# Optimization experiments

Measured on AMD Instinct MI355X. Metric: run time of the kernel, lower is better.

## Reference

```python
import jax, jax.numpy as jnp
import numpy as np

CHUNK = 32  # config.scan_chunk_size


def setup_inputs() -> dict:
    key = jax.random.key(0)
    ks = jax.random.split(key, 12)
    B, T, D, SD, OD = 8, 2048, 512, 256, 64
    w = lambda i, shape: (jax.random.normal(ks[i], shape, dtype=jnp.float32) * 0.02)
    return {
        "x": jax.random.normal(ks[0], (B, T, D), dtype=jnp.float32),
        "gate_W": w(1, (D, SD)), "gate_b": jnp.zeros((SD,), jnp.float32),
        "in_W": w(2, (D, SD)), "in_b": jnp.zeros((SD,), jnp.float32),
        "out_W": w(3, (SD, D)), "out_b": jnp.zeros((D,), jnp.float32),
        "opv_W": w(4, (D, OD)), "opv_b": jnp.zeros((OD,), jnp.float32),
        "opk_W": w(5, (D, OD)), "opk_b": jnp.zeros((OD,), jnp.float32),
        "opq_W": w(6, (D, OD)), "opq_b": jnp.zeros((OD,), jnp.float32),
        "op_decay": jnp.full((OD,), 0.95, jnp.float32),
        "opout_W": w(7, (OD, D)), "opout_b": jnp.zeros((D,), jnp.float32),
        "ln_g": jnp.ones((D,), jnp.float32), "ln_b": jnp.zeros((D,), jnp.float32),
    }


def _chunked_scan(gates, drive, K):
    # gates, drive: [B,T,SD]; T divisible by K
    B, T, SD = drive.shape
    nC = T // K
    a = gates.reshape(B, nC, K, SD)
    b = drive.reshape(B, nC, K, SD)
    log_cum_a = jnp.cumsum(jnp.log(jnp.maximum(a, 1e-6)), axis=2)
    cum_a = jnp.exp(log_cum_a)                               # [B,nC,K,SD]
    cum_wb = jnp.cumsum(b / jnp.maximum(cum_a, 1e-8), axis=2)
    # sequential scan over chunks to propagate the carry h
    def step(h, inputs):
        ca_last, wb_last = inputs                            # [B,SD] each
        h_new = ca_last * (h + wb_last)
        return h_new, h                                      # emit h BEFORE this chunk
    h0 = jnp.zeros((B, SD), drive.dtype)
    _, h_prev = jax.lax.scan(
        step, h0,
        (cum_a[:, :, -1].transpose(1, 0, 2), cum_wb[:, :, -1].transpose(1, 0, 2)))
    h_prev = h_prev.transpose(1, 0, 2)                       # [B,nC,SD]
    states = cum_a * (h_prev[:, :, None, :] + cum_wb)
    return states.reshape(B, T, SD)


def _binding_scan_outer(v, k, q, decay):
    # v,k,q: [B,T,OD]; S_t = diag(decay) @ S_{t-1} + v_t k_t^T; o_t = S_t q_t
    B, T, OD = v.shape
    def step(S, vkq):
        vt, kt, qt = vkq                                     # [B,OD] each
        S_new = decay[None, :, None] * S + vt[:, :, None] * kt[:, None, :]
        o = jnp.einsum('bij,bj->bi', S_new, qt)
        return S_new, o
    S0 = jnp.zeros((B, OD, OD), v.dtype)
    _, outs = jax.lax.scan(step, S0, (v.transpose(1, 0, 2), k.transpose(1, 0, 2), q.transpose(1, 0, 2)))
    return outs.transpose(1, 0, 2)                           # [B,T,OD]


def reference(x, gate_W, gate_b, in_W, in_b, out_W, out_b,
              opv_W, opv_b, opk_W, opk_b, opq_W, opq_b, op_decay,
              opout_W, opout_b, ln_g, ln_b):
    gates = jax.nn.sigmoid(x @ gate_W + gate_b)              # [B,T,SD]
    drive = (1.0 - gates) * (x @ in_W + in_b)
    states = _chunked_scan(gates, drive, CHUNK)
    scan_out = states @ out_W + out_b                        # [B,T,D]
    # binding scan (mode='outer')
    v = x @ opv_W + opv_b
    k = x @ opk_W + opk_b
    q = x @ opq_W + opq_b
    dec = jax.nn.sigmoid(op_decay)
    bind = _binding_scan_outer(v, k, q, dec) @ opout_W + opout_b
    y = x + scan_out + bind
    mu = jnp.mean(y, axis=-1, keepdims=True)
    var = jnp.mean((y - mu) ** 2, axis=-1, keepdims=True)
    return (y - mu) / jnp.sqrt(var + 1e-5) * ln_g + ln_b
```

## Files before the change

### kernel.cpp

```cpp
#include <hip/hip_runtime.h>
#include <hip/hip_bf16.h>
#include <hip/hip_fp16.h>
#include <math.h>

#define BB 8
#define TT 2048
#define DD 512
#define SD 256
#define OD 64
#define CHUNK 32
#define NC 64
#define CB 64
#define NCB 32
#define MM (BB*TT)
#define KCAT 320

typedef __attribute__((ext_vector_type(8))) short bf16x8_t;
typedef __attribute__((ext_vector_type(4))) float f32x4;

__device__ __forceinline__ void gload_lds16(const void* gsrc, void* ldst) {
    __builtin_amdgcn_global_load_lds(
        (const __attribute__((address_space(1))) unsigned int*)gsrc,
        (__attribute__((address_space(3))) unsigned int*)ldst,
        16, 0, 0);
}

__device__ __forceinline__ float4 ldh4(const __half* p) {
    __half2 a = *(const __half2*)p;
    __half2 b = *(const __half2*)(p + 2);
    float2 fa = __half22float2(a), fb = __half22float2(b);
    return make_float4(fa.x, fa.y, fb.x, fb.y);
}

__global__ __launch_bounds__(256) void conv_w(
    const float* __restrict__ gate_W, const float* __restrict__ gate_b,
    const float* __restrict__ in_W,   const float* __restrict__ in_b,
    const float* __restrict__ opv_W,  const float* __restrict__ opk_W,
    const float* __restrict__ opq_W,
    const float* __restrict__ opv_b,  const float* __restrict__ opk_b,
    const float* __restrict__ opq_b,
    const float* __restrict__ out_W,  const float* __restrict__ out_b,
    const float* __restrict__ opout_W, const float* __restrict__ opout_b,
    __hip_bfloat16* __restrict__ Wcat,  __hip_bfloat16* __restrict__ Wcomb,
    float* __restrict__ bias_cat, float* __restrict__ bias_comb)
{
    int idx = blockIdx.x * 256 + threadIdx.x;
    if (idx < 393216) {
        int n = idx >> 9, k = idx & 511;
        float v;
        if (n < 256)       v = gate_W[k * 256 + n];
        else if (n < 512)  v = in_W[k * 256 + (n - 256)];
        else if (n < 704) {
            int h = (n - 512) >> 6, j = (n - 512) & 63;
            const float* W = (h == 0) ? opv_W : (h == 1) ? opk_W : opq_W;
            v = W[k * 64 + j];
        } else v = 0.f;
        Wcat[idx] = __float2bfloat16(v);
        return;
    }
    idx -= 393216;
    if (idx < 163840) {
        int n = idx / KCAT, k = idx % KCAT;
        float v = (k < 256) ? out_W[k * 512 + n] : opout_W[(k - 256) * 512 + n];
        Wcomb[idx] = __float2bfloat16(v);
        return;
    }
    idx -= 163840;
    if (idx < 768) {
        float v;
        if (idx < 256)      v = gate_b[idx];
        else if (idx < 512) v = in_b[idx - 256];
        else if (idx < 704) {
            int h = (idx - 512) >> 6, j = (idx - 512) & 63;
            v = (h == 0) ? opv_b[j] : (h == 1) ? opk_b[j] : opq_b[j];
        } else v = 0.f;
        bias_cat[idx] = v;
        return;
    }
    idx -= 768;
    if (idx < 512) bias_comb[idx] = out_b[idx] + opout_b[idx];
}

__global__ __launch_bounds__(512, 6) void gemm_proj(
    const float* __restrict__ A,
    const __hip_bfloat16* __restrict__ Bt,
    const float* __restrict__ bias,
    __half* __restrict__ out0,
    __half* __restrict__ out1,
    int M, int N, int K, int n0, int sigCols)
{
    constexpr int BM = 128, BK = 32;
    __shared__ alignas(16) __hip_bfloat16 As[2][BM * BK];
    __shared__ alignas(16) __hip_bfloat16 Bs[2][BM * BK];
    const int tid = threadIdx.x;
    const int lane = tid & 63, wid = tid >> 6;
    const int wr = wid >> 2, wc = wid & 3;
    const int nbn = N >> 7;
    const int chunk = gridDim.x >> 3;
    const int b = blockIdx.x;
    const int orig = (b & 7) * chunk + (b >> 3);
    const int bm = (orig / nbn) * BM, bn = (orig % nbn) * BM;
    const int l15 = lane & 15, hgr = lane >> 4;

    const int grow = tid >> 2, gslot = tid & 3;
    const int gsw = gslot ^ ((grow >> 1) & 3);
    const float* srcA = A + (size_t)(bm + grow) * K + gslot * 8;
    const int wOffA = grow * 64 + gsw * 16;
    const __hip_bfloat16* srcB = Bt + (size_t)(bn + grow) * K + gsw * 8;
    const int ldsOffB = (tid & ~63) * 16;

    int offA[4], offB[2];
    #pragma unroll
    for (int mi = 0; mi < 4; ++mi) {
        int r = wr * 64 + mi * 16 + l15;
        offA[mi] = r * 64 + (hgr ^ ((r >> 1) & 3)) * 16;
    }
    #pragma unroll
    for (int nj = 0; nj < 2; ++nj) {
        int r = wc * 32 + nj * 16 + l15;
        offB[nj] = r * 64 + (hgr ^ ((r >> 1) & 3)) * 16;
    }

    f32x4 acc[4][2] = {};
    const int nk = K / BK;
    float4 a4lo, a4hi;

    a4lo = *(const float4*)(srcA);
    a4hi = *(const float4*)(srcA + 4);
    gload_lds16(srcB, (char*)&Bs[0][0] + ldsOffB);
    {
        alignas(16) __hip_bfloat16 h[8] = {
            __float2bfloat16(a4lo.x), __float2bfloat16(a4lo.y),
            __float2bfloat16(a4lo.z), __float2bfloat16(a4lo.w),
            __float2bfloat16(a4hi.x), __float2bfloat16(a4hi.y),
            __float2bfloat16(a4hi.z), __float2bfloat16(a4hi.w)};
        *(float4*)((char*)&As[0][0] + wOffA) = *(float4*)h;
    }
    __syncthreads();

    int cur = 0;
    for (int t = 0; t < nk; ++t) {
        const bool more = (t + 1 < nk);
        if (more) {
            int k0 = (t + 1) * BK;
            a4lo = *(const float4*)(srcA + k0);
            a4hi = *(const float4*)(srcA + k0 + 4);
            gload_lds16(srcB + k0, (char*)&Bs[cur ^ 1][0] + ldsOffB);
        }
        bf16x8_t af[4], bfr[2];
        #pragma unroll
        for (int mi = 0; mi < 4; ++mi)
            af[mi] = *(const bf16x8_t*)((const char*)&As[cur][0] + offA[mi]);
        #pragma unroll
        for (int nj = 0; nj < 2; ++nj)
            bfr[nj] = *(const bf16x8_t*)((const char*)&Bs[cur][0] + offB[nj]);
        #pragma unroll
        for (int mi = 0; mi < 4; ++mi)
            #pragma unroll
            for (int nj = 0; nj < 2; ++nj)
                acc[mi][nj] = __builtin_amdgcn_mfma_f32_16x16x32_bf16(
                    af[mi], bfr[nj], acc[mi][nj], 0, 0, 0);
        if (more) {
            alignas(16) __hip_bfloat16 h[8] = {
                __float2bfloat16(a4lo.x), __float2bfloat16(a4lo.y),
                __float2bfloat16(a4lo.z), __float2bfloat16(a4lo.w),
                __float2bfloat16(a4hi.x), __float2bfloat16(a4hi.y),
                __float2bfloat16(a4hi.z), __float2bfloat16(a4hi.w)};
            *(float4*)((char*)&As[cur ^ 1][0] + wOffA) = *(float4*)h;
        }
        __syncthreads();
        cur ^= 1;
    }

    const int n1 = N - n0;
    #pragma unroll
    for (int mi = 0; mi < 4; ++mi) {
        #pragma unroll
        for (int nj = 0; nj < 2; ++nj) {
            int col = bn + wc * 32 + nj * 16 + l15;
            int r0 = bm + wr * 64 + mi * 16 + hgr * 4;
            float bv = bias[col];
            #pragma unroll
            for (int e = 0; e < 4; ++e) {
                int row = r0 + e;
                float val = acc[mi][nj][e] + bv;
                if (col < n0) {
                    if (col < sigCols) val = 1.f / (1.f + expf(-val));
                    out0[(size_t)row * n0 + col] = __float2half(val);
                } else {
                    out1[(size_t)row * n1 + (col - n0)] = __float2half(val);
                }
            }
        }
    }
}

__device__ void scan_pass1_body(int blk,
    const __half* __restrict__ gi,
    float* __restrict__ ca_last, float* __restrict__ wb_last)
{
    int idx = blk * 256 + threadIdx.x;
    int sd = idx & 255;
    int c  = (idx >> 8) & 63;
    int b  = idx >> 14;
    size_t base = ((size_t)(b * TT + c * CHUNK)) * 512;
    float prod = 1.f, wb = 0.f;
    for (int i = 0; i < CHUNK; ++i) {
        size_t off = base + (size_t)i * 512;
        float g  = __half2float(gi[off + sd]);
        float il = __half2float(gi[off + 256 + sd]);
        float a = fmaxf(g, 1e-6f);
        prod *= a;
        wb += (1.f - g) * il / fmaxf(prod, 1e-8f);
    }
    int cidx = (b * NC + c) * SD + sd;
    ca_last[cidx] = prod;
    wb_last[cidx] = wb;
}

__device__ void scan_pass3_body(int blk,
    const __half* __restrict__ gi, const float* __restrict__ h_prev,
    __hip_bfloat16* __restrict__ cat)
{
    int idx = blk * 256 + threadIdx.x;
    int sd = idx & 255;
    int c  = (idx >> 8) & 63;
    int b  = idx >> 14;
    size_t base = ((size_t)(b * TT + c * CHUNK)) * 512;
    size_t obase = ((size_t)(b * TT + c * CHUNK)) * KCAT + sd;
    float h = h_prev[(b * NC + c) * SD + sd];
    float prod = 1.f, wb = 0.f;
    for (int i = 0; i < CHUNK; ++i) {
        size_t off = base + (size_t)i * 512;
        float g  = __half2float(gi[off + sd]);
        float il = __half2float(gi[off + 256 + sd]);
        float a = fmaxf(g, 1e-6f);
        prod *= a;
        wb += (1.f - g) * il / fmaxf(prod, 1e-8f);
        cat[obase + (size_t)i * KCAT] = __float2bfloat16(prod * (h + wb));
    }
}

#define LST 68
__device__ void bind_p1_body(int bc,
    const __half* __restrict__ vkq, const float* __restrict__ op_decay,
    float* __restrict__ o, float* __restrict__ dS,
    float* B1, float* B2, float* B3, float* l2d)
{
    const int b = bc >> 5, c = bc & 31;
    const size_t base = ((size_t)b * TT + (size_t)c * CB) * 256;
    const size_t obase = ((size_t)b * TT + (size_t)c * CB) * OD;
    const int tid = threadIdx.x;
    if (tid < 64) l2d[tid] = log2f(1.f / (1.f + expf(-op_decay[tid])));
    const int lr = tid >> 4, lc = (tid & 15) << 2;
    #pragma unroll
    for (int rr = 0; rr < 4; ++rr) {
        int t = lr + rr * 16;
        float4 qv = ldh4(&vkq[base + t * 256 + 128 + lc]);
        float4 kv = ldh4(&vkq[base + t * 256 + 64 + lc]);
        float q4[4] = {qv.x, qv.y, qv.z, qv.w};
        float k4[4] = {kv.x, kv.y, kv.z, kv.w};
        #pragma unroll
        for (int j = 0; j < 4; ++j) {
            B1[(lc + j) * LST + t] = q4[j];
            B2[(lc + j) * LST + t] = k4[j];
        }
    }
    __syncthreads();
    const int tx = tid & 15, ty = tid >> 4;
    {
        float a_acc[4][4] = {};
        for (int d = 0; d < 64; ++d) {
            float4 q4 = *(const float4*)&B1[d * LST + 4 * ty];
            float4 k4 = *(const float4*)&B2[d * LST + 4 * tx];
            float qr[4] = {q4.x, q4.y, q4.z, q4.w};
            float kr[4] = {k4.x, k4.y, k4.z, k4.w};
            #pragma unroll
            for (int r = 0; r < 4; ++r)
                #pragma unroll
                for (int s = 0; s < 4; ++s)
                    a_acc[r][s] = fmaf(qr[r], kr[s], a_acc[r][s]);
        }
        __syncthreads();
        #pragma unroll
        for (int s = 0; s < 4; ++s) {
            int ss = 4 * tx + s;
            float w[4];
            #pragma unroll
            for (int r = 0; r < 4; ++r)
                w[r] = (ss <= 4 * ty + r) ? a_acc[r][s] : 0.f;
            *(float4*)&B3[ss * LST + 4 * ty] = *(float4*)w;
        }
    }
    #pragma unroll
    for (int rr = 0; rr < 4; ++rr) {
        int m = lr + rr * 16;
        float4 vv = ldh4(&vkq[base + m * 256 + 0 + lc]);
        float4 kv = ldh4(&vkq[base + m * 256 + 64 + lc]);
        float v4[4] = {vv.x, vv.y, vv.z, vv.w};
        #pragma unroll
        for (int j = 0; j < 4; ++j)
            v4[j] *= exp2f(-(float)m * l2d[lc + j]);
        *(float4*)&B1[m * LST + lc] = *(float4*)v4;
        float k4[4] = {kv.x, kv.y, kv.z, kv.w};
        *(float4*)&B2[m * LST + lc] = *(float4*)k4;
    }
    __syncthreads();
    {
        float p[4][4] = {};
        for (int s = 0; s < 64; ++s) {
            float4 a4 = *(const float4*)&B3[s * LST + 4 * ty];
            float4 v4 = *(const float4*)&B1[s * LST + 4 * tx];
            float ar[4] = {a4.x, a4.y, a4.z, a4.w};
            float vr[4] = {v4.x, v4.y, v4.z, v4.w};
            #pragma unroll
            for (int r = 0; r < 4; ++r)
                #pragma unroll
                for (int i2 = 0; i2 < 4; ++i2)
                    p[r][i2] = fmaf(ar[r], vr[i2], p[r][i2]);
        }
        #pragma unroll
        for (int r = 0; r < 4; ++r) {
            int t = 4 * ty + r;
            float w[4];
            #pragma unroll
            for (int i2 = 0; i2 < 4; ++i2)
                w[i2] = exp2f((float)t * l2d[4 * tx + i2]) * p[r][i2];
            *(float4*)&o[obase + t * OD + 4 * tx] = *(float4*)w;
        }
    }
    {
        float sacc[4][4] = {};
        for (int m = 0; m < 64; ++m) {
            float4 v4 = *(const float4*)&B1[m * LST + 4 * ty];
            float4 k4 = *(const float4*)&B2[m * LST + 4 * tx];
            float vr[4] = {v4.x, v4.y, v4.z, v4.w};
            float kr[4] = {k4.x, k4.y, k4.z, k4.w};
            #pragma unroll
            for (int r = 0; r < 4; ++r)
                #pragma unroll
                for (int j = 0; j < 4; ++j)
                    sacc[r][j] = fmaf(vr[r], kr[j], sacc[r][j]);
        }
        float* dSb = dS + (size_t)bc * 4096;
        #pragma unroll
        for (int r = 0; r < 4; ++r) {
            int i = 4 * ty + r;
            float scale = exp2f(63.f * l2d[i]);
            float w[4];
            #pragma unroll
            for (int j2 = 0; j2 < 4; ++j2)
                w[j2] = scale * sacc[r][j2];
            *(float4*)&dSb[i * 64 + 4 * tx] = *(float4*)w;
        }
    }
}

__device__ void bind_p3_body(int bc,
    const __half* __restrict__ vkq, const float* __restrict__ Sstart,
    const float* __restrict__ op_decay, const float* __restrict__ o,
    __hip_bfloat16* __restrict__ cat,
    float* B1, float* B2, float* l2d)
{
    const int b = bc >> 5, c = bc & 31;
    const size_t base = ((size_t)b * TT + (size_t)c * CB) * 256;
    const size_t obase = ((size_t)b * TT + (size_t)c * CB) * OD;
    const size_t cbase = ((size_t)b * TT + (size_t)c * CB) * KCAT + 256;
    const int tid = threadIdx.x;
    if (tid < 64) l2d[tid] = log2f(1.f / (1.f + expf(-op_decay[tid])));
    const int lr = tid >> 4, lc = (tid & 15) << 2;
    const float* Sb = Sstart + (size_t)bc * 4096;
    #pragma unroll
    for (int rr = 0; rr < 4; ++rr) {
        int t = lr + rr * 16;
        float4 qv = ldh4(&vkq[base + t * 256 + 128 + lc]);
        float4 sv = *(const float4*)&Sb[t * 64 + lc];
        float q4[4] = {qv.x, qv.y, qv.z, qv.w};
        float s4[4] = {sv.x, sv.y, sv.z, sv.w};
        #pragma unroll
        for (int j = 0; j < 4; ++j) {
            B1[(lc + j) * LST + t] = q4[j];
            B2[(lc + j) * LST + t] = s4[j];
        }
    }
    __syncthreads();
    const int tx = tid & 15, ty = tid >> 4;
    float acc[4][4] = {};
    for (int j = 0; j < 64; ++j) {
        float4 q4 = *(const float4*)&B1[j * LST + 4 * ty];
        float4 s4 = *(const float4*)&B2[j * LST + 4 * tx];
        float qr[4] = {q4.x, q4.y, q4.z, q4.w};
        float sr[4] = {s4.x, s4.y, s4.z, s4.w};
        #pragma unroll
        for (int r = 0; r < 4; ++r)
            #pragma unroll
            for (int i2 = 0; i2 < 4; ++i2)
                acc[r][i2] = fmaf(qr[r], sr[i2], acc[r][i2]);
    }
    #pragma unroll
    for (int r = 0; r < 4; ++r) {
        int l = 4 * ty + r;
        alignas(8) __hip_bfloat16 w[4];
        #pragma unroll
        for (int i2 = 0; i2 < 4; ++i2) {
            int i = 4 * tx + i2;
            float val = o[obase + l * OD + i] + exp2f((float)(l + 1) * l2d[i]) * acc[r][i2];
            w[i2] = __float2bfloat16(val);
        }
        *(float2*)&cat[cbase + l * KCAT + 4 * tx] = *(float2*)w;
    }
}

__global__ __launch_bounds__(256) void fused1(
    const __half* __restrict__ gi, const __half* __restrict__ vkq,
    const float* __restrict__ op_decay,
    float* __restrict__ ca_last, float* __restrict__ wb_last,
    float* __restrict__ o_intra, float* __restrict__ dS)
{
    __shared__ float B1[64 * LST];
    __shared__ float B2[64 * LST];
    __shared__ float B3[64 * LST];
    __shared__ float l2d[64];
    const int bid = blockIdx.x;
    if (bid < 256) bind_p1_body(bid, vkq, op_decay, o_intra, dS, B1, B2, B3, l2d);
    else           scan_pass1_body(bid - 256, gi, ca_last, wb_last);
}

__global__ __launch_bounds__(256) void fused2(
    const float* __restrict__ dS, const float* __restrict__ op_decay,
    float* __restrict__ Sstart,
    const float* __restrict__ ca_last, const float* __restrict__ wb_last,
    float* __restrict__ h_prev)
{
    const int bid = blockIdx.x;
    if (bid < 128) {
        int idx = bid * 256 + threadIdx.x;
        int j = idx & 63, i = (idx >> 6) & 63, b = idx >> 12;
        float dec = 1.f / (1.f + expf(-op_decay[i]));
        float d64 = exp2f(64.f * log2f(dec));
        float S = 0.f;
        for (int c = 0; c < NCB; ++c) {
            size_t o = (((size_t)b * NCB + c) * 4096) + i * 64 + j;
            Sstart[o] = S;
            S = d64 * S + dS[o];
        }
    } else {
        int idx = (bid - 128) * 256 + threadIdx.x;
        int sd = idx & 255;
        int b  = idx >> 8;
        float h = 0.f;
        for (int c = 0; c < NC; ++c) {
            int o = (b * NC + c) * SD + sd;
            h_prev[o] = h;
            h = ca_last[o] * (h + wb_last[o]);
        }
    }
}

__global__ __launch_bounds__(256) void fused3(
    const __half* __restrict__ gi, const float* __restrict__ h_prev,
    const __half* __restrict__ vkq, const float* __restrict__ Sstart,
    const float* __restrict__ op_decay, const float* __restrict__ o_intra,
    __hip_bfloat16* __restrict__ cat)
{
    __shared__ float B1[64 * LST];
    __shared__ float B2[64 * LST];
    __shared__ float l2d[64];
    const int bid = blockIdx.x;
    if (bid < 256) bind_p3_body(bid, vkq, Sstart, op_decay, o_intra, cat, B1, B2, l2d);
    else           scan_pass3_body(bid - 256, gi, h_prev, cat);
}

__global__ __launch_bounds__(512) void outgemm_ln(
    const __hip_bfloat16* __restrict__ cat,
    const __hip_bfloat16* __restrict__ Wcomb,
    const float* __restrict__ bias_comb,
    const float* __restrict__ x,
    const float* __restrict__ lng, const float* __restrict__ lnb,
    float* __restrict__ y)
{
    constexpr int BM = 32, BK = 32, NN = 512;
    __shared__ alignas(16) __hip_bfloat16 As[2][BM * BK];
    __shared__ alignas(16) __hip_bfloat16 Bs[2][NN * BK];
    __shared__ float psum[8][BM], psum2[8][BM], mvmu[BM], mvrs[BM];
    const int tid = threadIdx.x;
    const int lane = tid & 63, wid = tid >> 6;
    const int l15 = lane & 15, hgr = lane >> 4;
    const int bm = blockIdx.x * BM;

    const __hip_bfloat16* srcA = cat;
    int ldsOffA = 0;
    {
        int gg = (wid & 1) * 64 + lane;
        int row = gg >> 2, sl = (gg & 3) ^ ((row >> 1) & 3);
        srcA = cat + (size_t)(bm + row) * KCAT + sl * 8;
        ldsOffA = (wid & 1) * 1024;
    }
    const __hip_bfloat16* srcB[4];
    int ldsOffB[4];
    #pragma unroll
    for (int c = 0; c < 4; ++c) {
        int gg = (wid * 4 + c) * 64 + lane;
        int row = gg >> 2, sl = (gg & 3) ^ ((row >> 1) & 3);
        srcB[c] = Wcomb + (size_t)row * KCAT + sl * 8;
        ldsOffB[c] = (wid * 4 + c) * 1024;
    }
    int offA[2], offB[4];
    #pragma unroll
    for (int mi = 0; mi < 2; ++mi) {
        int r = mi * 16 + l15;
        offA[mi] = r * 64 + (hgr ^ ((r >> 1) & 3)) * 16;
    }
    #pragma unroll
    for (int nj = 0; nj < 4; ++nj) {
        int n = wid * 64 + nj * 16 + l15;
        offB[nj] = n * 64 + (hgr ^ ((n >> 1) & 3)) * 16;
    }

    f32x4 acc[2][4] = {};
    constexpr int nk = KCAT / BK;

    if (wid < 2) gload_lds16(srcA, (char*)&As[0][0] + ldsOffA);
    #pragma unroll
    for (int c = 0; c < 4; ++c) gload_lds16(srcB[c], (char*)&Bs[0][0] + ldsOffB[c]);
    __syncthreads();

    int cur = 0;
    for (int t = 0; t < nk; ++t) {
        if (t + 1 < nk) {
            int k0 = (t + 1) * BK;
            if (wid < 2) gload_lds16(srcA + k0, (char*)&As[cur ^ 1][0] + ldsOffA);
            #pragma unroll
            for (int c = 0; c < 4; ++c)
                gload_lds16(srcB[c] + k0, (char*)&Bs[cur ^ 1][0] + ldsOffB[c]);
        }
        bf16x8_t af[2], bfr[4];
        #pragma unroll
        for (int mi = 0; mi < 2; ++mi)
            af[mi] = *(const bf16x8_t*)((const char*)&As[cur][0] + offA[mi]);
        #pragma unroll
        for (int nj = 0; nj < 4; ++nj)
            bfr[nj] = *(const bf16x8_t*)((const char*)&Bs[cur][0] + offB[nj]);
        #pragma unroll
        for (int mi = 0; mi < 2; ++mi)
            #pragma unroll
            for (int nj = 0; nj < 4; ++nj)
                acc[mi][nj] = __builtin_amdgcn_mfma_f32_16x16x32_bf16(
                    af[mi], bfr[nj], acc[mi][nj], 0, 0, 0);
        __syncthreads();
        cur ^= 1;
    }

    #pragma unroll
    for (int nj = 0; nj < 4; ++nj) {
        int col = wid * 64 + nj * 16 + l15;
        float bc_ = bias_comb[col];
        #pragma unroll
        for (int mi = 0; mi < 2; ++mi) {
            int r0 = bm + mi * 16 + hgr * 4;
            #pragma unroll
            for (int e = 0; e < 4; ++e)
                acc[mi][nj][e] += bc_ + x[(size_t)(r0 + e) * DD + col];
        }
    }
    float s[8], s2[8];
    #pragma unroll
    for (int mi = 0; mi < 2; ++mi)
        #pragma unroll
        for (int e = 0; e < 4; ++e) {
            float a = 0.f, b2 = 0.f;
            #pragma unroll
            for (int nj = 0; nj < 4; ++nj) {
                float v = acc[mi][nj][e];
                a += v; b2 += v * v;
            }
            s[mi * 4 + e] = a; s2[mi * 4 + e] = b2;
        }
    #pragma unroll
    for (int off = 1; off <= 8; off <<= 1)
        #pragma unroll
        for (int i = 0; i < 8; ++i) {
            s[i]  += __shfl_xor(s[i], off);
            s2[i] += __shfl_xor(s2[i], off);
        }
    if (l15 == 0) {
        #pragma unroll
        for (int mi = 0; mi < 2; ++mi)
            #pragma unroll
            for (int e = 0; e < 4; ++e) {
                int lr = mi * 16 + hgr * 4 + e;
                psum[wid][lr]  = s[mi * 4 + e];
                psum2[wid][lr] = s2[mi * 4 + e];
            }
    }
    __syncthreads();
    if (tid < BM) {
        float tot = 0.f, tot2 = 0.f;
        #pragma unroll
        for (int w2 = 0; w2 < 8; ++w2) { tot += psum[w2][tid]; tot2 += psum2[w2][tid]; }
        float mu = tot * (1.f / 512.f);
        float var = tot2 * (1.f / 512.f) - mu * mu;
        mvmu[tid] = mu;
        mvrs[tid] = rsqrtf(var + 1e-5f);
    }
    __syncthreads();
    #pragma unroll
    for (int nj = 0; nj < 4; ++nj) {
        int col = wid * 64 + nj * 16 + l15;
        float g = lng[col], bb = lnb[col];
        #pragma unroll
        for (int mi = 0; mi < 2; ++mi) {
            #pragma unroll
            for (int e = 0; e < 4; ++e) {
                int lr = mi * 16 + hgr * 4 + e;
                y[(size_t)(bm + lr) * DD + col] =
                    (acc[mi][nj][e] - mvmu[lr]) * mvrs[lr] * g + bb;
            }
        }
    }
}

extern "C" void kernel_launch(void* const* d_in, const int* in_sizes, int n_in,
                              void* d_out, int out_size, void* d_ws, size_t ws_size,
                              hipStream_t stream)
{
    const float* x       = (const float*)d_in[0];
    const float* gate_W  = (const float*)d_in[1];
    const float* gate_b  = (const float*)d_in[2];
    const float* in_W    = (const float*)d_in[3];
    const float* in_b    = (const float*)d_in[4];
    const float* out_W   = (const float*)d_in[5];
    const float* out_b   = (const float*)d_in[6];
    const float* opv_W   = (const float*)d_in[7];
    const float* opv_b   = (const float*)d_in[8];
    const float* opk_W   = (const float*)d_in[9];
    const float* opk_b   = (const float*)d_in[10];
    const float* opq_W   = (const float*)d_in[11];
    const float* opq_b   = (const float*)d_in[12];
    const float* op_dec  = (const float*)d_in[13];
    const float* opout_W = (const float*)d_in[14];
    const float* opout_b = (const float*)d_in[15];
    const float* ln_g    = (const float*)d_in[16];
    const float* ln_b    = (const float*)d_in[17];
    float* y = (float*)d_out;

    char* w = (char*)d_ws;
    auto alloc = [&](size_t bytes) { char* p = w; w += (bytes + 255) & ~(size_t)255; return p; };
    __half* gi       = (__half*)alloc((size_t)MM * 512 * 2);
    __half* vkq      = (__half*)alloc((size_t)MM * 256 * 2);
    float* o_intra   = (float*)alloc((size_t)MM * 64 * 4);
    float* ca_last   = (float*)alloc((size_t)BB * NC * SD * 4);
    float* wb_last   = (float*)alloc((size_t)BB * NC * SD * 4);
    float* h_prev    = (float*)alloc((size_t)BB * NC * SD * 4);
    float* dS        = (float*)alloc((size_t)BB * NCB * 4096 * 4);
    float* Sstart    = (float*)alloc((size_t)BB * NCB * 4096 * 4);
    float* bias_cat  = (float*)alloc(768 * 4);
    float* bias_comb = (float*)alloc(512 * 4);
    __hip_bfloat16* cat   = (__hip_bfloat16*)alloc((size_t)MM * KCAT * 2);
    __hip_bfloat16* Wcat  = (__hip_bfloat16*)alloc((size_t)768 * 512 * 2);
    __hip_bfloat16* Wcomb = (__hip_bfloat16*)alloc((size_t)512 * KCAT * 2);

    hipLaunchKernelGGL(conv_w, dim3((393216 + 163840 + 768 + 512 + 255) / 256), dim3(256), 0, stream,
                       gate_W, gate_b, in_W, in_b, opv_W, opk_W, opq_W,
                       opv_b, opk_b, opq_b, out_W, out_b, opout_W, opout_b,
                       Wcat, Wcomb, bias_cat, bias_comb);
    hipLaunchKernelGGL(gemm_proj, dim3(6 * (MM / 128)), dim3(512), 0, stream,
                       x, Wcat, bias_cat, gi, vkq,
                       MM, 768, 512, 512, 256);
    hipLaunchKernelGGL(fused1, dim3(768), dim3(256), 0, stream,
                       gi, vkq, op_dec, ca_last, wb_last, o_intra, dS);
    hipLaunchKernelGGL(fused2, dim3(136), dim3(256), 0, stream,
                       dS, op_dec, Sstart, ca_last, wb_last, h_prev);
    hipLaunchKernelGGL(fused3, dim3(768), dim3(256), 0, stream,
                       gi, h_prev, vkq, Sstart, op_dec, o_intra, cat);
    hipLaunchKernelGGL(outgemm_ln, dim3(MM / 32), dim3(512), 0, stream,
                       cat, Wcomb, bias_comb, x, ln_g, ln_b, y);
}
```

Measured before the change: 87.77 us.

## Triple-buffer projection GEMM with two-stage-ahead prefetch and manual waitcnt

Rewrites the gemm_proj main loop from double-buffered to triple-buffered LDS, issuing global loads two k-steps ahead. Explicit vmcnt/lgkmcnt waits and raw s_barrier with sched barriers replace __syncthreads, so outstanding loads for the next tile are not drained at each barrier. The goal is to hide global memory latency behind the MFMA work. The cost is more LDS per block, which may lower occupancy under the 6-block launch bound, plus fragile hand-counted wait values and a loop that assumes nk is even and at least 4.

New measurement: 87.36 us. About the same (-0.5%).

```diff
diff --git a/kernel.cpp b/kernel.cpp
--- a/kernel.cpp
+++ b/kernel.cpp
@@ -90,8 +90,8 @@
     int M, int N, int K, int n0, int sigCols)
 {
     constexpr int BM = 128, BK = 32;
-    __shared__ alignas(16) __hip_bfloat16 As[2][BM * BK];
-    __shared__ alignas(16) __hip_bfloat16 Bs[2][BM * BK];
+    __shared__ alignas(16) __hip_bfloat16 Abuf[3][BM * BK];
+    __shared__ alignas(16) __hip_bfloat16 Bbuf[3][BM * BK];
     const int tid = threadIdx.x;
     const int lane = tid & 63, wid = tid >> 6;
     const int wr = wid >> 2, wc = wid & 3;
@@ -123,54 +123,71 @@
 
     f32x4 acc[4][2] = {};
     const int nk = K / BK;
-    float4 a4lo, a4hi;
-
-    a4lo = *(const float4*)(srcA);
-    a4hi = *(const float4*)(srcA + 4);
-    gload_lds16(srcB, (char*)&Bs[0][0] + ldsOffB);
-    {
-        alignas(16) __hip_bfloat16 h[8] = {
-            __float2bfloat16(a4lo.x), __float2bfloat16(a4lo.y),
-            __float2bfloat16(a4lo.z), __float2bfloat16(a4lo.w),
-            __float2bfloat16(a4hi.x), __float2bfloat16(a4hi.y),
-            __float2bfloat16(a4hi.z), __float2bfloat16(a4hi.w)};
-        *(float4*)((char*)&As[0][0] + wOffA) = *(float4*)h;
-    }
+    float4 pA0, pA1, qA0, qA1;
+
+#define WRITE_A(IDX, R0, R1) do { \
+        alignas(16) __hip_bfloat16 h_[8] = { \
+            __float2bfloat16((R0).x), __float2bfloat16((R0).y), \
+            __float2bfloat16((R0).z), __float2bfloat16((R0).w), \
+            __float2bfloat16((R1).x), __float2bfloat16((R1).y), \
+            __float2bfloat16((R1).z), __float2bfloat16((R1).w)}; \
+        *(float4*)((char*)&Abuf[(IDX)][0] + wOffA) = *(float4*)h_; \
+    } while (0)
+
+#define FRAG_MFMA(T) do { \
+        const char* ab_ = (const char*)&Abuf[(T) % 3][0]; \
+        const char* bb_ = (const char*)&Bbuf[(T) % 3][0]; \
+        bf16x8_t af_[4], bf_[2]; \
+        _Pragma("unroll") \
+        for (int mi = 0; mi < 4; ++mi) af_[mi] = *(const bf16x8_t*)(ab_ + offA[mi]); \
+        _Pragma("unroll") \
+        for (int nj = 0; nj < 2; ++nj) bf_[nj] = *(const bf16x8_t*)(bb_ + offB[nj]); \
+        _Pragma("unroll") \
+        for (int mi = 0; mi < 4; ++mi) \
+            _Pragma("unroll") \
+            for (int nj = 0; nj < 2; ++nj) \
+                acc[mi][nj] = __builtin_amdgcn_mfma_f32_16x16x32_bf16( \
+                    af_[mi], bf_[nj], acc[mi][nj], 0, 0, 0); \
+    } while (0)
+
+#define GEMM_STEP(T, I0, I1, W0, W1) do { \
+        int k2_ = ((T) + 2) * BK; \
+        I0 = *(const float4*)(srcA + k2_); \
+        I1 = *(const float4*)(srcA + k2_ + 4); \
+        gload_lds16(srcB + k2_, (char*)&Bbuf[((T) + 2) % 3][0] + ldsOffB); \
+        FRAG_MFMA(T); \
+        WRITE_A(((T) + 1) % 3, W0, W1); \
+        asm volatile("s_waitcnt vmcnt(3) lgkmcnt(0)" ::: "memory"); \
+        __builtin_amdgcn_sched_barrier(0); \
+        __builtin_amdgcn_s_barrier(); \
+        __builtin_amdgcn_sched_barrier(0); \
+    } while (0)
+
+    pA0 = *(const float4*)(srcA);
+    pA1 = *(const float4*)(srcA + 4);
+    gload_lds16(srcB, (char*)&Bbuf[0][0] + ldsOffB);
+    qA0 = *(const float4*)(srcA + BK);
+    qA1 = *(const float4*)(srcA + BK + 4);
+    gload_lds16(srcB + BK, (char*)&Bbuf[1][0] + ldsOffB);
+    asm volatile("s_waitcnt vmcnt(3)" ::: "memory");
+    WRITE_A(0, pA0, pA1);
+    asm volatile("s_waitcnt lgkmcnt(0)" ::: "memory");
+    __builtin_amdgcn_sched_barrier(0);
+    __builtin_amdgcn_s_barrier();
+    __builtin_amdgcn_sched_barrier(0);
+
+    for (int tt = 0; tt + 3 < nk; tt += 2) {
+        GEMM_STEP(tt,     pA0, pA1, qA0, qA1);
+        GEMM_STEP(tt + 1, qA0, qA1, pA0, pA1);
+    }
+    FRAG_MFMA(nk - 2);
+    WRITE_A((nk - 1) % 3, qA0, qA1);
     __syncthreads();
-
-    int cur = 0;
-    for (int t = 0; t < nk; ++t) {
-        const bool more = (t + 1 < nk);
-        if (more) {
-            int k0 = (t + 1) * BK;
-            a4lo = *(const float4*)(srcA + k0);
-            a4hi = *(const float4*)(srcA + k0 + 4);
-            gload_lds16(srcB + k0, (char*)&Bs[cur ^ 1][0] + ldsOffB);
-        }
-        bf16x8_t af[4], bfr[2];
-        #pragma unroll
-        for (int mi = 0; mi < 4; ++mi)
-            af[mi] = *(const bf16x8_t*)((const char*)&As[cur][0] + offA[mi]);
-        #pragma unroll
-        for (int nj = 0; nj < 2; ++nj)
-            bfr[nj] = *(const bf16x8_t*)((const char*)&Bs[cur][0] + offB[nj]);
-        #pragma unroll
-        for (int mi = 0; mi < 4; ++mi)
-            #pragma unroll
-            for (int nj = 0; nj < 2; ++nj)
-                acc[mi][nj] = __builtin_amdgcn_mfma_f32_16x16x32_bf16(
-                    af[mi], bfr[nj], acc[mi][nj], 0, 0, 0);
-        if (more) {
-            alignas(16) __hip_bfloat16 h[8] = {
-                __float2bfloat16(a4lo.x), __float2bfloat16(a4lo.y),
-                __float2bfloat16(a4lo.z), __float2bfloat16(a4lo.w),
-                __float2bfloat16(a4hi.x), __float2bfloat16(a4hi.y),
-                __float2bfloat16(a4hi.z), __float2bfloat16(a4hi.w)};
-            *(float4*)((char*)&As[cur ^ 1][0] + wOffA) = *(float4*)h;
-        }
-        __syncthreads();
-        cur ^= 1;
-    }
+    FRAG_MFMA(nk - 1);
+
+#undef GEMM_STEP
+#undef FRAG_MFMA
+#undef WRITE_A
 
     const int n1 = N - n0;
     #pragma unroll
```
